# Performance work log

Hardware: AMD Instinct MI355X
Metric: run time of the kernel (lower is better)

Reference implementation:

```python
import jax, jax.numpy as jnp
import numpy as np
import math

B, S, D, H, DH = 2, 4096, 1024, 16, 64
CHUNK, RNDS, NBUCK, MLP = 128, 2, 64, 4096


def setup_inputs() -> dict:
    key = jax.random.key(0)
    ks = jax.random.split(key, 8)
    return {
        "inputs": jax.random.normal(ks[0], (B, S, D), jnp.float32),
        "ln1_scale": jnp.ones((D,), jnp.float32),
        "ln1_bias": jnp.zeros((D,), jnp.float32),
        "w_qk": jax.random.normal(ks[1], (D, H, DH), jnp.float32) * 0.02,
        "w_v": jax.random.normal(ks[2], (D, H, DH), jnp.float32) * 0.02,
        "w_out": jax.random.normal(ks[3], (H, DH, D), jnp.float32) * 0.02,
        "rotations": jax.random.normal(ks[4], (DH, RNDS, NBUCK // 2), jnp.float32),
        "ln2_scale": jnp.ones((D,), jnp.float32),
        "ln2_bias": jnp.zeros((D,), jnp.float32),
        "w_mlp1": jax.random.normal(ks[5], (D, MLP), jnp.float32) * 0.02,
        "b_mlp1": jnp.zeros((MLP,), jnp.float32),
        "w_mlp2": jax.random.normal(ks[6], (MLP, D), jnp.float32) * 0.02,
        "b_mlp2": jnp.zeros((D,), jnp.float32),
    }


def _layer_norm(x, scale, bias):
    mu = x.mean(-1, keepdims=True)
    var = ((x - mu) ** 2).mean(-1, keepdims=True)
    return (x - mu) / jnp.sqrt(var + 1e-6) * scale + bias


def _attend_one(q, k, v, buckets):
    # q,k,v: [S,DH]; buckets: [S] int. Sort by bucket (stable via position tiebreak),
    # chunk, attend to own chunk + 1 before + 1 after (look_both_side).
    nC = S // CHUNK
    order = jnp.argsort(buckets * S + jnp.arange(S))  # [S]
    undo = jnp.argsort(order)
    sq = q[order].reshape(nC, CHUNK, DH)
    sk = k[order].reshape(nC, CHUNK, DH)
    sv = v[order].reshape(nC, CHUNK, DH)
    st = order.reshape(nC, CHUNK)  # original token positions
    look = lambda x: jnp.concatenate([x, jnp.roll(x, 1, axis=0), jnp.roll(x, -1, axis=0)], axis=1)
    bk, bv = look(sk), look(sv)
    bt = look(st[..., None])[..., 0]
    dots = jnp.einsum('nqd,nkd->nqk', sq, bk) / math.sqrt(DH)
    # self_mask: a token attends to itself only if nothing else is available
    dots = dots - 1e5 * (st[:, :, None] == bt[:, None, :]).astype(dots.dtype)
    slog = jax.nn.logsumexp(dots, axis=-1)           # [nC,CHUNK]
    o = jnp.einsum('nqk,nkd->nqd', jax.nn.softmax(dots, axis=-1), bv)
    return o.reshape(S, DH)[undo], slog.reshape(S)[undo]


def _lsh_attention(qk, v, rotations):
    # qk,v: [B,H,S,DH]; shared-QK Reformer attention; keys are length-normalized.
    xn = qk / (jnp.linalg.norm(qk, axis=-1, keepdims=True) + 1e-6)
    rot = jnp.einsum('bhsd,drm->bhrsm', xn, rotations)          # [B,H,R,S,NBUCK/2]
    buckets = jnp.argmax(jnp.concatenate([rot, -rot], -1), -1)  # [B,H,R,S]
    rep = lambda x: jnp.broadcast_to(x[:, :, None], (B, H, RNDS, S, DH)).reshape(-1, S, DH)
    o, slog = jax.vmap(_attend_one)(rep(qk), rep(xn), rep(v), buckets.reshape(-1, S))
    o = o.reshape(B, H, RNDS, S, DH)
    slog = slog.reshape(B, H, RNDS, S)
    w = jax.nn.softmax(slog, axis=2)  # combine hash rounds by their logsumexp weight
    return (o * w[..., None]).sum(axis=2)  # [B,H,S,DH]


def reference(inputs, ln1_scale, ln1_bias, w_qk, w_v, w_out, rotations,
              ln2_scale, ln2_bias, w_mlp1, b_mlp1, w_mlp2, b_mlp2):
    x = _layer_norm(inputs, ln1_scale, ln1_bias)
    qk = jnp.einsum('bsd,dhe->bhse', x, w_qk)
    v = jnp.einsum('bsd,dhe->bhse', x, w_v)
    att = _lsh_attention(qk, v, rotations)
    x2 = inputs + jnp.einsum('bhse,hed->bsd', att, w_out)
    y = _layer_norm(x2, ln2_scale, ln2_bias)
    y = jax.nn.gelu(y @ w_mlp1 + b_mlp1) @ w_mlp2 + b_mlp2
    return x2 + y
```

## Files before the change

kernel.cpp:

```cpp
#include <hip/hip_runtime.h>
#include <hip/hip_bf16.h>


typedef short short8 __attribute__((ext_vector_type(8)));
typedef float f32x4 __attribute__((ext_vector_type(4)));
typedef unsigned short us4 __attribute__((ext_vector_type(4)));

__device__ __forceinline__ unsigned short f2bf(float f) {
  unsigned u = __builtin_bit_cast(unsigned, f);
  u += 0x7FFFu + ((u >> 16) & 1u);
  return (unsigned short)(u >> 16);
}

__device__ __forceinline__ float bf2f(unsigned short u) {
  return __builtin_bit_cast(float, ((unsigned)u) << 16);
}

__device__ __forceinline__ float gelu_f(float x) {
  float x3 = x * x * x;
  float t = tanhf(0.7978845608028654f * (x + 0.044715f * x3));
  return 0.5f * x * (1.0f + t);
}

__device__ __forceinline__ void load_lds16(const void* g, void* l) {
  __builtin_amdgcn_global_load_lds(
      (const __attribute__((address_space(1))) unsigned int*)g,
      (__attribute__((address_space(3))) unsigned int*)l, 16, 0, 0);
}

__global__ __launch_bounds__(256) void transpose_cast(
    const float* __restrict__ in, unsigned short* __restrict__ out, int R,
    int C) {
  __shared__ float tile[32][33];
  int ctiles = C >> 5;
  int bx = blockIdx.x % ctiles;
  int by = blockIdx.x / ctiles;
  int tx = threadIdx.x & 31;
  int ty = threadIdx.x >> 5;
#pragma unroll
  for (int i = 0; i < 32; i += 8)
    tile[ty + i][tx] = in[(size_t)(by * 32 + ty + i) * C + bx * 32 + tx];
  __syncthreads();
#pragma unroll
  for (int i = 0; i < 32; i += 8)
    out[(size_t)(bx * 32 + ty + i) * R + by * 32 + tx] = f2bf(tile[tx][ty + i]);
}

__global__ __launch_bounds__(256) void ln_bf16(const float* __restrict__ x,
                                               const float* __restrict__ sc,
                                               const float* __restrict__ bi,
                                               unsigned short* __restrict__ y) {
  int row = blockIdx.x, tid = threadIdx.x, lane = tid & 63, wv = tid >> 6;
  const float* xr = x + (size_t)row * 1024;
  float4 v = *(const float4*)(xr + tid * 4);
  float s1 = v.x + v.y + v.z + v.w;
  float s2 = v.x * v.x + v.y * v.y + v.z * v.z + v.w * v.w;
#pragma unroll
  for (int o = 1; o < 64; o <<= 1) {
    s1 += __shfl_xor(s1, o);
    s2 += __shfl_xor(s2, o);
  }
  __shared__ float a1[4], a2[4];
  if (lane == 0) {
    a1[wv] = s1;
    a2[wv] = s2;
  }
  __syncthreads();
  s1 = a1[0] + a1[1] + a1[2] + a1[3];
  s2 = a2[0] + a2[1] + a2[2] + a2[3];
  float mu = s1 * (1.f / 1024.f);
  float var = s2 * (1.f / 1024.f) - mu * mu;
  float rs = rsqrtf(var + 1e-6f);
  int c = tid * 4;
  us4 o4;
  o4.x = f2bf((v.x - mu) * rs * sc[c + 0] + bi[c + 0]);
  o4.y = f2bf((v.y - mu) * rs * sc[c + 1] + bi[c + 1]);
  o4.z = f2bf((v.z - mu) * rs * sc[c + 2] + bi[c + 2]);
  o4.w = f2bf((v.w - mu) * rs * sc[c + 3] + bi[c + 3]);
  *(us4*)(y + (size_t)row * 1024 + c) = o4;
}


template <int BK, int EPI>
__global__ __launch_bounds__(256) void gemm_bt(
    const unsigned short* __restrict__ A, const unsigned short* __restrict__ Bt,
    const float* __restrict__ bias, const float* __restrict__ res,
    float* __restrict__ Cf, unsigned short* __restrict__ Cb,
    unsigned short* __restrict__ Cb2, int M, int N, int K) {
  constexpr int GR = BK / 8;
  constexpr int RPS = 2048 / BK;
  constexpr int LPM = BK / 16;

  __shared__ unsigned short sA[2][128 * BK];
  __shared__ unsigned short sB[2][128 * BK];

  const int nbx = N / 128;
  const int nwg = gridDim.x;
  const int cpx = nwg >> 3;
  const int bid = blockIdx.x;
  const int swz = (bid & 7) * cpx + (bid >> 3);
  const int bx = swz % nbx;
  const int by = swz / nbx;
  const int tid = threadIdx.x;
  const int lane = tid & 63;
  const int wave = tid >> 6;
  const int wr = wave >> 1, wc = wave & 1;
  const int l15 = lane & 15;
  const int lhi = lane >> 4;

  const int srow = tid / GR;
  const int swzrow = (BK == 32) ? ((srow >> 1) & 3) : (srow & 7);
  const int sgl = (tid % GR) ^ swzrow;
  const unsigned short* Ag = A + (size_t)(by * 128 + srow) * K + sgl * 8;
  const unsigned short* Bg = Bt + (size_t)(bx * 128 + srow) * K + sgl * 8;

  f32x4 acc[4][4];
#pragma unroll
  for (int m = 0; m < 4; ++m)
#pragma unroll
    for (int n = 0; n < 4; ++n) {
      f32x4 z = {0.f, 0.f, 0.f, 0.f};
      acc[m][n] = z;
    }

  const int KT = K / BK;

  auto STAGE = [&](int ktile, int buf) {
    const unsigned short* As = Ag + (size_t)ktile * BK;
    const unsigned short* Bs = Bg + (size_t)ktile * BK;
#pragma unroll
    for (int i = 0; i < LPM; ++i) {
      load_lds16(As + (size_t)i * RPS * K,
                 (char*)&sA[buf][0] + tid * 16 + i * 4096);
      load_lds16(Bs + (size_t)i * RPS * K,
                 (char*)&sB[buf][0] + tid * 16 + i * 4096);
    }
  };

  STAGE(0, 0);
  __syncthreads();

  int cur = 0;
  const int arow = wr * 64 + l15;
  const int brow = wc * 64 + l15;

  for (int kt = 0; kt < KT; ++kt) {
    if (kt + 1 < KT) STAGE(kt + 1, cur ^ 1);
#pragma unroll
    for (int ks = 0; ks < BK / 32; ++ks) {
      const int physg =
          (BK == 32) ? (lhi ^ ((l15 >> 1) & 3)) : ((ks * 4 + lhi) ^ (l15 & 7));
      const int koff = physg * 8;
      short8 af[4], bfv[4];
#pragma unroll
      for (int m = 0; m < 4; ++m)
        af[m] = *(const short8*)&sA[cur][(arow + m * 16) * BK + koff];
#pragma unroll
      for (int n = 0; n < 4; ++n)
        bfv[n] = *(const short8*)&sB[cur][(brow + n * 16) * BK + koff];
#pragma unroll
      for (int m = 0; m < 4; ++m)
#pragma unroll
        for (int n = 0; n < 4; ++n)
          acc[m][n] = __builtin_amdgcn_mfma_f32_16x16x32_bf16(
              af[m], bfv[n], acc[m][n], 0, 0, 0);
    }
    __syncthreads();
    cur ^= 1;
  }

  const int r0 = by * 128 + wr * 64;
  const int c0 = bx * 128 + wc * 64;
#pragma unroll
  for (int m = 0; m < 4; ++m) {
#pragma unroll
    for (int n = 0; n < 4; ++n) {
#pragma unroll
      for (int i = 0; i < 4; ++i) {
        int rr = r0 + m * 16 + lhi * 4 + i;
        int cc = c0 + n * 16 + l15;
        float vacc = acc[m][n][i];
        if (EPI == 1) {
          float t = vacc + bias[cc];
          Cb[(size_t)rr * N + cc] = f2bf(gelu_f(t));
        } else if (EPI == 2) {
          float t = vacc + res[(size_t)rr * N + cc];
          if (bias != nullptr) t += bias[cc];
          Cf[(size_t)rr * N + cc] = t;
        } else if (EPI == 5) {
          if (cc < 1024) {
            Cf[(size_t)rr * 1024 + cc] = vacc;
            Cb[(size_t)rr * 1024 + cc] = f2bf(vacc);
          } else {
            Cb2[(size_t)rr * 1024 + (cc - 1024)] = f2bf(vacc);
          }
        }
      }
    }
  }
}

__global__ __launch_bounds__(256) void bucket_kernel(
    const float* __restrict__ qk, const float* __restrict__ rot,
    unsigned short* __restrict__ knb, int* __restrict__ buckets) {
  __shared__ float rotl[64 * 64];
  __shared__ float xnl[4][64];
  int tid = threadIdx.x, lane = tid & 63, wv = tid >> 6;
  for (int i = tid; i < 4096; i += 256) rotl[i] = rot[i];
  __syncthreads();
  for (int it = 0; it < 8; ++it) {
    int g = (it * 4096 + blockIdx.x) * 4 + wv;
    int bh = g >> 12;
    int s = g & 4095;
    int b = bh >> 4, h = bh & 15;
    size_t rowoff = (size_t)(b * 4096 + s) * 1024 + h * 64;
    float x = qk[rowoff + lane];
    float ss = x * x;
#pragma unroll
    for (int o = 1; o < 64; o <<= 1) ss += __shfl_xor(ss, o);
    float rn = 1.f / (sqrtf(ss) + 1e-6f);
    float xn = x * rn;
    knb[rowoff + lane] = f2bf(xn);
    xnl[wv][lane] = xn;
    __syncthreads();
    int r_ = lane >> 5, m_ = lane & 31;
    float a = 0.f;
#pragma unroll 16
    for (int d = 0; d < 64; ++d) a += xnl[wv][d] * rotl[d * 64 + r_ * 32 + m_];
    float bv;
    int bi;
    if (a >= 0.f) {
      bv = a;
      bi = m_;
    } else {
      bv = -a;
      bi = m_ + 32;
    }
#pragma unroll
    for (int o = 16; o >= 1; o >>= 1) {
      float ov = __shfl_xor(bv, o);
      int oi = __shfl_xor(bi, o);
      if (ov > bv || (ov == bv && oi < bi)) {
        bv = ov;
        bi = oi;
      }
    }
    if (m_ == 0) buckets[((size_t)bh * 2 + r_) * 4096 + s] = bi;
    __syncthreads();
  }
}

#define HSTR 65

__global__ __launch_bounds__(256) void sort_kernel(
    const int* __restrict__ buckets, int* __restrict__ order) {
  __shared__ unsigned int hist[256 * HSTR];
  __shared__ unsigned int bucketStart[64];
  const int bhr = blockIdx.x;
  const int t = threadIdx.x;
  const int* bk = buckets + (size_t)bhr * 4096;

  unsigned int* hrow = &hist[t * HSTR];
#pragma unroll
  for (int b = 0; b < 64; ++b) hrow[b] = 0u;

  int bks[16];
  {
    const int4* bp = (const int4*)(bk + t * 16);
#pragma unroll
    for (int j4 = 0; j4 < 4; ++j4) {
      int4 v = bp[j4];
      bks[j4 * 4 + 0] = v.x;
      bks[j4 * 4 + 1] = v.y;
      bks[j4 * 4 + 2] = v.z;
      bks[j4 * 4 + 3] = v.w;
    }
  }
#pragma unroll
  for (int j = 0; j < 16; ++j) hrow[bks[j]]++;
  __syncthreads();

  if (t < 64) {
    unsigned int acc = 0;
    for (int t2 = 0; t2 < 256; ++t2) {
      unsigned int c = hist[t2 * HSTR + t];
      hist[t2 * HSTR + t] = acc;
      acc += c;
    }
    bucketStart[t] = acc;
  }
  __syncthreads();
  if (t == 0) {
    unsigned int acc = 0;
    for (int b = 0; b < 64; ++b) {
      unsigned int c = bucketStart[b];
      bucketStart[b] = acc;
      acc += c;
    }
  }
  __syncthreads();

  int* op = order + (size_t)bhr * 4096;
#pragma unroll
  for (int j = 0; j < 16; ++j) {
    int b = bks[j];
    unsigned int pos = bucketStart[b] + hrow[b];
    hrow[b]++;
    op[pos] = t * 16 + j;
  }
}

#define KSTR 72
#define PSTR 136

__global__ __launch_bounds__(256, 2) void lsh_attn_mfma(
    const unsigned short* __restrict__ qb, const unsigned short* __restrict__ knb,
    const unsigned short* __restrict__ vb, const int* __restrict__ order,
    unsigned short* __restrict__ ob, float* __restrict__ slog) {
  __shared__ unsigned short Kls[128 * KSTR];
  __shared__ unsigned short Vt[64 * PSTR];
  __shared__ unsigned short Pls[4][32 * PSTR];
  __shared__ int qtokL[128];
  __shared__ int btok[128];

  const int bid = blockIdx.x;
  const int swz = (bid & 7) * 256 + (bid >> 3);
  const int c = swz & 31;
  const int bhr = swz >> 5;
  const int bh = bhr >> 1;
  const int h = bh & 15, b = bh >> 4;
  const int* ord = order + (size_t)bhr * 4096;
  const int tid = threadIdx.x, lane = tid & 63, wv = tid >> 6;
  const int l15 = lane & 15, lhi = lane >> 4;

  if (tid < 128) qtokL[tid] = ord[c * 128 + tid];
  __syncthreads();

  short8 qf[2][2];
#pragma unroll
  for (int mt = 0; mt < 2; ++mt) {
#pragma unroll
    for (int ks = 0; ks < 2; ++ks) {
      int tok = qtokL[wv * 32 + mt * 16 + l15];
      qf[mt][ks] = *(const short8*)(qb + (size_t)(b * 4096 + tok) * 1024 +
                                    h * 64 + ks * 32 + lhi * 8);
    }
  }

  float mrun[2][4], lrun[2][4];
  f32x4 oacc[2][4];
#pragma unroll
  for (int mt = 0; mt < 2; ++mt)
#pragma unroll
    for (int i = 0; i < 4; ++i) {
      mrun[mt][i] = -1e30f;
      lrun[mt][i] = 0.f;
    }
#pragma unroll
  for (int mt = 0; mt < 2; ++mt)
#pragma unroll
    for (int n = 0; n < 4; ++n) {
      f32x4 z = {0.f, 0.f, 0.f, 0.f};
      oacc[mt][n] = z;
    }

  for (int st = 0; st < 3; ++st) {
    int kc = (st == 0) ? c : (st == 1) ? ((c + 31) & 31) : ((c + 1) & 31);
    __syncthreads();
    {
      int row = tid >> 1, half = tid & 1;
      int ktok = ord[kc * 128 + row];
      if (half == 0) btok[row] = ktok;
      size_t rowoff = (size_t)(b * 4096 + ktok) * 1024 + h * 64 + half * 32;
      const short8* kp = (const short8*)(knb + rowoff);
      const short8* vp = (const short8*)(vb + rowoff);
#pragma unroll
      for (int i = 0; i < 4; ++i)
        *(short8*)&Kls[row * KSTR + half * 32 + i * 8] = kp[i];
#pragma unroll
      for (int i = 0; i < 4; ++i) {
        short8 vw = vp[i];
        int d0 = half * 32 + i * 8;
#pragma unroll
        for (int j = 0; j < 8; ++j)
          Vt[(d0 + j) * PSTR + row] = (unsigned short)vw[j];
      }
    }
    __syncthreads();

    f32x4 sacc[2][8];
#pragma unroll
    for (int mt = 0; mt < 2; ++mt)
#pragma unroll
      for (int n = 0; n < 8; ++n) {
        f32x4 z = {0.f, 0.f, 0.f, 0.f};
        sacc[mt][n] = z;
      }
#pragma unroll
    for (int ks = 0; ks < 2; ++ks) {
      short8 kf[8];
#pragma unroll
      for (int n = 0; n < 8; ++n)
        kf[n] = *(const short8*)&Kls[(n * 16 + l15) * KSTR + ks * 32 + lhi * 8];
#pragma unroll
      for (int mt = 0; mt < 2; ++mt)
#pragma unroll
        for (int n = 0; n < 8; ++n)
          sacc[mt][n] = __builtin_amdgcn_mfma_f32_16x16x32_bf16(
              qf[mt][ks], kf[n], sacc[mt][n], 0, 0, 0);
    }

    int ktA[8];
#pragma unroll
    for (int n = 0; n < 8; ++n) ktA[n] = btok[n * 16 + l15];
#pragma unroll
    for (int mt = 0; mt < 2; ++mt) {
#pragma unroll
      for (int i = 0; i < 4; ++i) {
        int qrow = wv * 32 + mt * 16 + lhi * 4 + i;
        int qt = qtokL[qrow];
        float sv[8];
        float mx = -1e30f;
#pragma unroll
        for (int n = 0; n < 8; ++n) {
          float s = sacc[mt][n][i] * 0.125f;
          if (ktA[n] == qt) s -= 1e5f;
          sv[n] = s;
          mx = fmaxf(mx, s);
        }
#pragma unroll
        for (int d = 1; d < 16; d <<= 1) mx = fmaxf(mx, __shfl_xor(mx, d));
        float mold = mrun[mt][i];
        float mnew = fmaxf(mold, mx);
        float scl = __expf(mold - mnew);
        lrun[mt][i] *= scl;
#pragma unroll
        for (int n = 0; n < 4; ++n) oacc[mt][n][i] *= scl;
        float ps = 0.f;
#pragma unroll
        for (int n = 0; n < 8; ++n) {
          float p = __expf(sv[n] - mnew);
          ps += p;
          Pls[wv][(mt * 16 + lhi * 4 + i) * PSTR + n * 16 + l15] = f2bf(p);
        }
#pragma unroll
        for (int d = 1; d < 16; d <<= 1) ps += __shfl_xor(ps, d);
        lrun[mt][i] = lrun[mt][i] + ps;
        mrun[mt][i] = mnew;
      }
    }

#pragma unroll
    for (int ks = 0; ks < 4; ++ks) {
      short8 pf[2];
#pragma unroll
      for (int mt = 0; mt < 2; ++mt)
        pf[mt] =
            *(const short8*)&Pls[wv][(mt * 16 + l15) * PSTR + ks * 32 + lhi * 8];
      short8 vfr[4];
#pragma unroll
      for (int n = 0; n < 4; ++n)
        vfr[n] = *(const short8*)&Vt[(n * 16 + l15) * PSTR + ks * 32 + lhi * 8];
#pragma unroll
      for (int mt = 0; mt < 2; ++mt)
#pragma unroll
        for (int n = 0; n < 4; ++n)
          oacc[mt][n] = __builtin_amdgcn_mfma_f32_16x16x32_bf16(
              pf[mt], vfr[n], oacc[mt][n], 0, 0, 0);
    }
  }

#pragma unroll
  for (int mt = 0; mt < 2; ++mt) {
#pragma unroll
    for (int i = 0; i < 4; ++i) {
      int qrow = wv * 32 + mt * 16 + lhi * 4 + i;
      int tok = qtokL[qrow];
      float l = lrun[mt][i];
      float invl = 1.f / l;
      if (l15 == 0) slog[(size_t)bhr * 4096 + tok] = logf(l) + mrun[mt][i];
      unsigned short* orow = ob + ((size_t)bhr * 4096 + tok) * 64;
#pragma unroll
      for (int n = 0; n < 4; ++n)
        orow[n * 16 + l15] = f2bf(oacc[mt][n][i] * invl);
    }
  }
}

__global__ __launch_bounds__(256) void combine_rounds(
    const unsigned short* __restrict__ ob, const float* __restrict__ slog,
    unsigned short* __restrict__ att) {
  int g = blockIdx.x * 4 + (threadIdx.x >> 6);
  int lane = threadIdx.x & 63;
  int h = g & 15;
  int bs = g >> 4;
  int b = bs >> 12;
  int s = bs & 4095;
  size_t base = ((size_t)(b * 16 + h) * 2) * 4096 + s;
  size_t i0 = base;
  size_t i1 = base + 4096;
  float s0 = slog[i0], s1 = slog[i1];
  float mx = fmaxf(s0, s1);
  float e0 = __expf(s0 - mx), e1 = __expf(s1 - mx);
  float w0 = e0 / (e0 + e1);
  float w1 = 1.f - w0;
  float v0 = bf2f(ob[i0 * 64 + lane]);
  float v1 = bf2f(ob[i1 * 64 + lane]);
  att[(size_t)bs * 1024 + h * 64 + lane] = f2bf(w0 * v0 + w1 * v1);
}

extern "C" void kernel_launch(void* const* d_in, const int* in_sizes, int n_in,
                              void* d_out, int out_size, void* d_ws,
                              size_t ws_size, hipStream_t stream) {
  const float* inputs = (const float*)d_in[0];
  const float* ln1s = (const float*)d_in[1];
  const float* ln1b = (const float*)d_in[2];
  const float* wqk = (const float*)d_in[3];
  const float* wv = (const float*)d_in[4];
  const float* wout = (const float*)d_in[5];
  const float* rot = (const float*)d_in[6];
  const float* ln2s = (const float*)d_in[7];
  const float* ln2b = (const float*)d_in[8];
  const float* wm1 = (const float*)d_in[9];
  const float* bm1 = (const float*)d_in[10];
  const float* wm2 = (const float*)d_in[11];
  const float* bm2 = (const float*)d_in[12];

  char* w = (char*)d_ws;
  auto alloc = [&](size_t bytes) {
    char* p = w;
    w += (bytes + 255) & ~(size_t)255;
    return p;
  };
  unsigned short* wqkv_bt = (unsigned short*)alloc(2048ull * 1024 * 2);
  unsigned short* wout_bt = (unsigned short*)alloc(1024ull * 1024 * 2);
  unsigned short* wm1_bt = (unsigned short*)alloc(4096ull * 1024 * 2);
  unsigned short* wm2_bt = (unsigned short*)alloc(1024ull * 4096 * 2);
  unsigned short* bufA = (unsigned short*)alloc(8192ull * 1024 * 2);
  float* qkf = (float*)alloc(8192ull * 1024 * 4);
  unsigned short* qb = (unsigned short*)alloc(8192ull * 1024 * 2);
  unsigned short* knb = (unsigned short*)alloc(8192ull * 1024 * 2);
  unsigned short* vb = (unsigned short*)alloc(8192ull * 1024 * 2);
  int* buckets = (int*)alloc(64ull * 4096 * 4);
  int* order = (int*)alloc(64ull * 4096 * 4);
  unsigned short* big =
      (unsigned short*)alloc(8192ull * 4096 * 2);
  float* slogb = (float*)alloc(64ull * 4096 * 4);
  float* x2 = qkf;
  unsigned short* obuf = big;
  unsigned short* h1 = big;

  transpose_cast<<<32 * 32, 256, 0, stream>>>(wqk, wqkv_bt, 1024, 1024);
  transpose_cast<<<32 * 32, 256, 0, stream>>>(wv, wqkv_bt + 1024ull * 1024,
                                              1024, 1024);
  transpose_cast<<<32 * 32, 256, 0, stream>>>(wout, wout_bt, 1024, 1024);
  transpose_cast<<<32 * 128, 256, 0, stream>>>(wm1, wm1_bt, 1024, 4096);
  transpose_cast<<<128 * 32, 256, 0, stream>>>(wm2, wm2_bt, 4096, 1024);

  ln_bf16<<<8192, 256, 0, stream>>>(inputs, ln1s, ln1b, bufA);

  gemm_bt<64, 5><<<64 * 16, 256, 0, stream>>>(bufA, wqkv_bt, nullptr, nullptr,
                                              qkf, qb, vb, 8192, 2048, 1024);

  bucket_kernel<<<4096, 256, 0, stream>>>(qkf, rot, knb, buckets);
  sort_kernel<<<64, 256, 0, stream>>>(buckets, order);
  lsh_attn_mfma<<<2048, 256, 0, stream>>>(qb, knb, vb, order, obuf, slogb);
  combine_rounds<<<32768, 256, 0, stream>>>(obuf, slogb, bufA);

  gemm_bt<64, 2><<<64 * 8, 256, 0, stream>>>(bufA, wout_bt, nullptr, inputs,
                                             x2, nullptr, nullptr, 8192, 1024,
                                             1024);
  ln_bf16<<<8192, 256, 0, stream>>>(x2, ln2s, ln2b, bufA);
  gemm_bt<32, 1><<<64 * 32, 256, 0, stream>>>(bufA, wm1_bt, bm1, nullptr,
                                              nullptr, h1, nullptr, 8192, 4096,
                                              1024);
  gemm_bt<64, 2><<<64 * 8, 256, 0, stream>>>(h1, wm2_bt, bm2, x2,
                                             (float*)d_out, nullptr, nullptr,
                                             8192, 1024, 4096);
}
```

Before: 497.8 us.

## Add phased-pipeline GEMM with split LDS reads and fine-grained waits

```diff
diff --git a/kernel.cpp b/kernel.cpp
--- a/kernel.cpp
+++ b/kernel.cpp
@@ -17,9 +17,8 @@
 }
 
 __device__ __forceinline__ float gelu_f(float x) {
-  float x3 = x * x * x;
-  float t = tanhf(0.7978845608028654f * (x + 0.044715f * x3));
-  return 0.5f * x * (1.0f + t);
+  float y = 1.5957691216057308f * (x + 0.044715f * x * x * x);
+  return x / (1.f + __expf(-y));
 }
 
 __device__ __forceinline__ void load_lds16(const void* g, void* l) {
@@ -80,20 +79,14 @@
   *(us4*)(y + (size_t)row * 1024 + c) = o4;
 }
 
-
-template <int BK, int EPI>
+template <int EPI>
 __global__ __launch_bounds__(256) void gemm_bt(
     const unsigned short* __restrict__ A, const unsigned short* __restrict__ Bt,
     const float* __restrict__ bias, const float* __restrict__ res,
-    float* __restrict__ Cf, unsigned short* __restrict__ Cb,
-    unsigned short* __restrict__ Cb2, int M, int N, int K) {
-  constexpr int GR = BK / 8;
-  constexpr int RPS = 2048 / BK;
-  constexpr int LPM = BK / 16;
-
-  __shared__ unsigned short sA[2][128 * BK];
-  __shared__ unsigned short sB[2][128 * BK];
-
+    float* __restrict__ Cf, unsigned short* __restrict__ Cb, int M, int N,
+    int K) {
+  __shared__ unsigned short sA[2][128 * 32];
+  __shared__ unsigned short sB[2][128 * 32];
   const int nbx = N / 128;
   const int nwg = gridDim.x;
   const int cpx = nwg >> 3;
@@ -108,9 +101,8 @@
   const int l15 = lane & 15;
   const int lhi = lane >> 4;
 
-  const int srow = tid / GR;
-  const int swzrow = (BK == 32) ? ((srow >> 1) & 3) : (srow & 7);
-  const int sgl = (tid % GR) ^ swzrow;
+  const int srow = tid >> 2;
+  const int sgl = (tid & 3) ^ ((srow >> 1) & 3);
   const unsigned short* Ag = A + (size_t)(by * 128 + srow) * K + sgl * 8;
   const unsigned short* Bg = Bt + (size_t)(bx * 128 + srow) * K + sgl * 8;
 
@@ -123,16 +115,16 @@
       acc[m][n] = z;
     }
 
-  const int KT = K / BK;
+  const int KT = K / 32;
 
   auto STAGE = [&](int ktile, int buf) {
-    const unsigned short* As = Ag + (size_t)ktile * BK;
-    const unsigned short* Bs = Bg + (size_t)ktile * BK;
-#pragma unroll
-    for (int i = 0; i < LPM; ++i) {
-      load_lds16(As + (size_t)i * RPS * K,
+    const unsigned short* As = Ag + (size_t)ktile * 32;
+    const unsigned short* Bs = Bg + (size_t)ktile * 32;
+#pragma unroll
+    for (int i = 0; i < 2; ++i) {
+      load_lds16(As + (size_t)i * 64 * K,
                  (char*)&sA[buf][0] + tid * 16 + i * 4096);
-      load_lds16(Bs + (size_t)i * RPS * K,
+      load_lds16(Bs + (size_t)i * 64 * K,
                  (char*)&sB[buf][0] + tid * 16 + i * 4096);
     }
   };
@@ -143,28 +135,23 @@
   int cur = 0;
   const int arow = wr * 64 + l15;
   const int brow = wc * 64 + l15;
+  const int koff = (lhi ^ ((l15 >> 1) & 3)) * 8;
 
   for (int kt = 0; kt < KT; ++kt) {
     if (kt + 1 < KT) STAGE(kt + 1, cur ^ 1);
-#pragma unroll
-    for (int ks = 0; ks < BK / 32; ++ks) {
-      const int physg =
-          (BK == 32) ? (lhi ^ ((l15 >> 1) & 3)) : ((ks * 4 + lhi) ^ (l15 & 7));
-      const int koff = physg * 8;
-      short8 af[4], bfv[4];
-#pragma unroll
-      for (int m = 0; m < 4; ++m)
-        af[m] = *(const short8*)&sA[cur][(arow + m * 16) * BK + koff];
+    short8 af[4], bfv[4];
+#pragma unroll
+    for (int m = 0; m < 4; ++m)
+      af[m] = *(const short8*)&sA[cur][(arow + m * 16) * 32 + koff];
+#pragma unroll
+    for (int n = 0; n < 4; ++n)
+      bfv[n] = *(const short8*)&sB[cur][(brow + n * 16) * 32 + koff];
+#pragma unroll
+    for (int m = 0; m < 4; ++m)
 #pragma unroll
       for (int n = 0; n < 4; ++n)
-        bfv[n] = *(const short8*)&sB[cur][(brow + n * 16) * BK + koff];
-#pragma unroll
-      for (int m = 0; m < 4; ++m)
-#pragma unroll
-        for (int n = 0; n < 4; ++n)
-          acc[m][n] = __builtin_amdgcn_mfma_f32_16x16x32_bf16(
-              af[m], bfv[n], acc[m][n], 0, 0, 0);
-    }
+        acc[m][n] = __builtin_amdgcn_mfma_f32_16x16x32_bf16(af[m], bfv[n],
+                                                            acc[m][n], 0, 0, 0);
     __syncthreads();
     cur ^= 1;
   }
@@ -184,6 +171,196 @@
           float t = vacc + bias[cc];
           Cb[(size_t)rr * N + cc] = f2bf(gelu_f(t));
         } else if (EPI == 2) {
+          float t = vacc + res[(size_t)rr * N + cc];
+          if (bias != nullptr) t += bias[cc];
+          Cf[(size_t)rr * N + cc] = t;
+        }
+      }
+    }
+  }
+}
+
+template <int EPI>
+__global__ __launch_bounds__(256) void gemm_p4(
+    const unsigned short* __restrict__ A, const unsigned short* __restrict__ Bt,
+    const float* __restrict__ bias, const float* __restrict__ res,
+    float* __restrict__ Cf, unsigned short* __restrict__ Cb,
+    unsigned short* __restrict__ Cb2, int M, int N, int K) {
+  __shared__ unsigned short sA[2][128 * 64];
+  __shared__ unsigned short sB[2][128 * 64];
+  const int nbx = N / 128;
+  const int nwg = gridDim.x;
+  const int cpx = nwg >> 3;
+  const int bid = blockIdx.x;
+  const int swz = (bid & 7) * cpx + (bid >> 3);
+  const int bx = swz % nbx;
+  const int by = swz / nbx;
+  const int tid = threadIdx.x;
+  const int lane = tid & 63;
+  const int wave = tid >> 6;
+  const int wr = wave >> 1, wc = wave & 1;
+  const int l15 = lane & 15;
+  const int lhi = lane >> 4;
+
+  const int r = tid >> 3;
+  const int g = tid & 7;
+  const int sgl = g ^ (r & 7);
+  const unsigned short* Ag = A + (size_t)(by * 128 + r) * K + sgl * 8;
+  const unsigned short* Bg = Bt + (size_t)(bx * 128 + r) * K + sgl * 8;
+  const int dst = tid * 16;
+
+  f32x4 acc[4][4];
+#pragma unroll
+  for (int m = 0; m < 4; ++m)
+#pragma unroll
+    for (int n = 0; n < 4; ++n) {
+      f32x4 z = {0.f, 0.f, 0.f, 0.f};
+      acc[m][n] = z;
+    }
+
+  const int KT = K / 64;
+
+  auto ISS = [&](int idx, int ktile, int buf) {
+    const int Rs = ((idx >> 2) << 5) + ((idx & 1) << 6);
+    const unsigned short* src =
+        ((idx & 2) ? Bg : Ag) + (size_t)Rs * K + (size_t)ktile * 64;
+    char* d = (char*)((idx & 2) ? &sB[buf][0] : &sA[buf][0]) + Rs * 128 + dst;
+    load_lds16(src, d);
+  };
+
+  const int arowb = wr * 64 + l15;
+  const int browb = wc * 64 + l15;
+  auto readA = [&](int m, int ks, int c) {
+    return *(const short8*)&sA[c][(arowb + m * 16) * 64 +
+                                  (((ks * 4 + lhi) ^ (l15 & 7)) << 3)];
+  };
+  auto readB = [&](int n, int ks, int c) {
+    return *(const short8*)&sB[c][(browb + n * 16) * 64 +
+                                  (((ks * 4 + lhi) ^ (l15 & 7)) << 3)];
+  };
+
+#define WAITV(N_) asm volatile("s_waitcnt vmcnt(" #N_ ")" ::: "memory")
+#define PHASE_SYNC()                              \
+  do {                                            \
+    __builtin_amdgcn_sched_barrier(0);            \
+    __builtin_amdgcn_s_barrier();                 \
+    asm volatile("s_waitcnt lgkmcnt(0)" ::: "memory"); \
+    __builtin_amdgcn_sched_barrier(0);            \
+  } while (0)
+
+#pragma unroll
+  for (int i = 0; i < 8; ++i) ISS(i, 0, 0);
+  WAITV(4);
+  __builtin_amdgcn_sched_barrier(0);
+  __builtin_amdgcn_s_barrier();
+
+  for (int kt = 0; kt < KT; ++kt) {
+    const int c = kt & 1;
+    const bool pre = (kt + 1 < KT);
+    short8 a0[2][2], a1[2][2], b0[2][2], b1[2][2];
+
+#pragma unroll
+    for (int i = 0; i < 2; ++i)
+#pragma unroll
+      for (int ks = 0; ks < 2; ++ks) {
+        a0[i][ks] = readA(i, ks, c);
+        b0[i][ks] = readB(i, ks, c);
+      }
+    if (pre) {
+      ISS(0, kt + 1, c ^ 1);
+      ISS(1, kt + 1, c ^ 1);
+      WAITV(4);
+    } else {
+      WAITV(2);
+    }
+    PHASE_SYNC();
+    __builtin_amdgcn_s_setprio(1);
+#pragma unroll
+    for (int i = 0; i < 2; ++i)
+#pragma unroll
+      for (int n = 0; n < 2; ++n)
+#pragma unroll
+        for (int ks = 0; ks < 2; ++ks)
+          acc[i][n] = __builtin_amdgcn_mfma_f32_16x16x32_bf16(
+              a0[i][ks], b0[n][ks], acc[i][n], 0, 0, 0);
+    __builtin_amdgcn_s_setprio(0);
+
+#pragma unroll
+    for (int i = 0; i < 2; ++i)
+#pragma unroll
+      for (int ks = 0; ks < 2; ++ks) a1[i][ks] = readA(2 + i, ks, c);
+    if (pre) {
+      ISS(2, kt + 1, c ^ 1);
+      ISS(3, kt + 1, c ^ 1);
+      WAITV(4);
+    } else {
+      WAITV(0);
+    }
+    PHASE_SYNC();
+    __builtin_amdgcn_s_setprio(1);
+#pragma unroll
+    for (int i = 0; i < 2; ++i)
+#pragma unroll
+      for (int n = 0; n < 2; ++n)
+#pragma unroll
+        for (int ks = 0; ks < 2; ++ks)
+          acc[2 + i][n] = __builtin_amdgcn_mfma_f32_16x16x32_bf16(
+              a1[i][ks], b0[n][ks], acc[2 + i][n], 0, 0, 0);
+    __builtin_amdgcn_s_setprio(0);
+
+#pragma unroll
+    for (int i = 0; i < 2; ++i)
+#pragma unroll
+      for (int ks = 0; ks < 2; ++ks) b1[i][ks] = readB(2 + i, ks, c);
+    if (pre) {
+      ISS(4, kt + 1, c ^ 1);
+      ISS(5, kt + 1, c ^ 1);
+      WAITV(4);
+    }
+    PHASE_SYNC();
+    __builtin_amdgcn_s_setprio(1);
+#pragma unroll
+    for (int i = 0; i < 2; ++i)
+#pragma unroll
+      for (int n = 0; n < 2; ++n)
+#pragma unroll
+        for (int ks = 0; ks < 2; ++ks)
+          acc[2 + i][2 + n] = __builtin_amdgcn_mfma_f32_16x16x32_bf16(
+              a1[i][ks], b1[n][ks], acc[2 + i][2 + n], 0, 0, 0);
+    __builtin_amdgcn_s_setprio(0);
+
+    if (pre) {
+      ISS(6, kt + 1, c ^ 1);
+      ISS(7, kt + 1, c ^ 1);
+      WAITV(4);
+    }
+    PHASE_SYNC();
+    __builtin_amdgcn_s_setprio(1);
+#pragma unroll
+    for (int i = 0; i < 2; ++i)
+#pragma unroll
+      for (int n = 0; n < 2; ++n)
+#pragma unroll
+        for (int ks = 0; ks < 2; ++ks)
+          acc[i][2 + n] = __builtin_amdgcn_mfma_f32_16x16x32_bf16(
+              a0[i][ks], b1[n][ks], acc[i][2 + n], 0, 0, 0);
+    __builtin_amdgcn_s_setprio(0);
+  }
+#undef WAITV
+#undef PHASE_SYNC
+
+  const int r0 = by * 128 + wr * 64;
+  const int c0 = bx * 128 + wc * 64;
+#pragma unroll
+  for (int m = 0; m < 4; ++m) {
+#pragma unroll
+    for (int n = 0; n < 4; ++n) {
+#pragma unroll
+      for (int i = 0; i < 4; ++i) {
+        int rr = r0 + m * 16 + lhi * 4 + i;
+        int cc = c0 + n * 16 + l15;
+        float vacc = acc[m][n][i];
+        if (EPI == 2) {
           float t = vacc + res[(size_t)rr * N + cc];
           if (bias != nullptr) t += bias[cc];
           Cf[(size_t)rr * N + cc] = t;
@@ -559,22 +736,19 @@
 
   ln_bf16<<<8192, 256, 0, stream>>>(inputs, ln1s, ln1b, bufA);
 
-  gemm_bt<64, 5><<<64 * 16, 256, 0, stream>>>(bufA, wqkv_bt, nullptr, nullptr,
-                                              qkf, qb, vb, 8192, 2048, 1024);
+  gemm_p4<5><<<64 * 16, 256, 0, stream>>>(bufA, wqkv_bt, nullptr, nullptr, qkf,
+                                          qb, vb, 8192, 2048, 1024);
 
   bucket_kernel<<<4096, 256, 0, stream>>>(qkf, rot, knb, buckets);
   sort_kernel<<<64, 256, 0, stream>>>(buckets, order);
   lsh_attn_mfma<<<2048, 256, 0, stream>>>(qb, knb, vb, order, obuf, slogb);
   combine_rounds<<<32768, 256, 0, stream>>>(obuf, slogb, bufA);
 
-  gemm_bt<64, 2><<<64 * 8, 256, 0, stream>>>(bufA, wout_bt, nullptr, inputs,
-                                             x2, nullptr, nullptr, 8192, 1024,
-                                             1024);
+  gemm_p4<2><<<64 * 8, 256, 0, stream>>>(bufA, wout_bt, nullptr, inputs, x2,
+                                         nullptr, nullptr, 8192, 1024, 1024);
   ln_bf16<<<8192, 256, 0, stream>>>(x2, ln2s, ln2b, bufA);
-  gemm_bt<32, 1><<<64 * 32, 256, 0, stream>>>(bufA, wm1_bt, bm1, nullptr,
-                                              nullptr, h1, nullptr, 8192, 4096,
-                                              1024);
-  gemm_bt<64, 2><<<64 * 8, 256, 0, stream>>>(h1, wm2_bt, bm2, x2,
-                                             (float*)d_out, nullptr, nullptr,
-                                             8192, 1024, 4096);
-}
+  gemm_bt<1><<<64 * 32, 256, 0, stream>>>(bufA, wm1_bt, bm1, nullptr, nullptr,
+                                          h1, 8192, 4096, 1024);
+  gemm_p4<2><<<64 * 8, 256, 0, stream>>>(h1, wm2_bt, bm2, x2, (float*)d_out,
+                                         nullptr, nullptr, 8192, 1024, 4096);
+}
```

New measurement: 514.6 us. 1.03x slower.

## Add 256x256 eight-wave GEMM with staged LDS prefetch for QKV and MLP1

Applied to the files above, without the earlier changes.

```diff
diff --git a/kernel.cpp b/kernel.cpp
--- a/kernel.cpp
+++ b/kernel.cpp
@@ -17,9 +17,8 @@
 }
 
 __device__ __forceinline__ float gelu_f(float x) {
-  float x3 = x * x * x;
-  float t = tanhf(0.7978845608028654f * (x + 0.044715f * x3));
-  return 0.5f * x * (1.0f + t);
+  float y = 1.5957691216057308f * (x + 0.044715f * x * x * x);
+  return x / (1.f + __expf(-y));
 }
 
 __device__ __forceinline__ void load_lds16(const void* g, void* l) {
@@ -80,20 +79,14 @@
   *(us4*)(y + (size_t)row * 1024 + c) = o4;
 }
 
-
-template <int BK, int EPI>
+template <int EPI>
 __global__ __launch_bounds__(256) void gemm_bt(
     const unsigned short* __restrict__ A, const unsigned short* __restrict__ Bt,
     const float* __restrict__ bias, const float* __restrict__ res,
-    float* __restrict__ Cf, unsigned short* __restrict__ Cb,
-    unsigned short* __restrict__ Cb2, int M, int N, int K) {
-  constexpr int GR = BK / 8;
-  constexpr int RPS = 2048 / BK;
-  constexpr int LPM = BK / 16;
-
-  __shared__ unsigned short sA[2][128 * BK];
-  __shared__ unsigned short sB[2][128 * BK];
-
+    float* __restrict__ Cf, unsigned short* __restrict__ Cb, int M, int N,
+    int K) {
+  __shared__ unsigned short sA[2][128 * 64];
+  __shared__ unsigned short sB[2][128 * 64];
   const int nbx = N / 128;
   const int nwg = gridDim.x;
   const int cpx = nwg >> 3;
@@ -108,9 +101,8 @@
   const int l15 = lane & 15;
   const int lhi = lane >> 4;
 
-  const int srow = tid / GR;
-  const int swzrow = (BK == 32) ? ((srow >> 1) & 3) : (srow & 7);
-  const int sgl = (tid % GR) ^ swzrow;
+  const int srow = tid >> 3;
+  const int sgl = (tid & 7) ^ (srow & 7);
   const unsigned short* Ag = A + (size_t)(by * 128 + srow) * K + sgl * 8;
   const unsigned short* Bg = Bt + (size_t)(bx * 128 + srow) * K + sgl * 8;
 
@@ -123,16 +115,16 @@
       acc[m][n] = z;
     }
 
-  const int KT = K / BK;
+  const int KT = K / 64;
 
   auto STAGE = [&](int ktile, int buf) {
-    const unsigned short* As = Ag + (size_t)ktile * BK;
-    const unsigned short* Bs = Bg + (size_t)ktile * BK;
-#pragma unroll
-    for (int i = 0; i < LPM; ++i) {
-      load_lds16(As + (size_t)i * RPS * K,
+    const unsigned short* As = Ag + (size_t)ktile * 64;
+    const unsigned short* Bs = Bg + (size_t)ktile * 64;
+#pragma unroll
+    for (int i = 0; i < 4; ++i) {
+      load_lds16(As + (size_t)i * 32 * K,
                  (char*)&sA[buf][0] + tid * 16 + i * 4096);
-      load_lds16(Bs + (size_t)i * RPS * K,
+      load_lds16(Bs + (size_t)i * 32 * K,
                  (char*)&sB[buf][0] + tid * 16 + i * 4096);
     }
   };
@@ -147,17 +139,15 @@
   for (int kt = 0; kt < KT; ++kt) {
     if (kt + 1 < KT) STAGE(kt + 1, cur ^ 1);
 #pragma unroll
-    for (int ks = 0; ks < BK / 32; ++ks) {
-      const int physg =
-          (BK == 32) ? (lhi ^ ((l15 >> 1) & 3)) : ((ks * 4 + lhi) ^ (l15 & 7));
-      const int koff = physg * 8;
+    for (int ks = 0; ks < 2; ++ks) {
+      const int koff = (((ks * 4 + lhi) ^ (l15 & 7)) << 3);
       short8 af[4], bfv[4];
 #pragma unroll
       for (int m = 0; m < 4; ++m)
-        af[m] = *(const short8*)&sA[cur][(arow + m * 16) * BK + koff];
+        af[m] = *(const short8*)&sA[cur][(arow + m * 16) * 64 + koff];
 #pragma unroll
       for (int n = 0; n < 4; ++n)
-        bfv[n] = *(const short8*)&sB[cur][(brow + n * 16) * BK + koff];
+        bfv[n] = *(const short8*)&sB[cur][(brow + n * 16) * 64 + koff];
 #pragma unroll
       for (int m = 0; m < 4; ++m)
 #pragma unroll
@@ -180,13 +170,194 @@
         int rr = r0 + m * 16 + lhi * 4 + i;
         int cc = c0 + n * 16 + l15;
         float vacc = acc[m][n][i];
-        if (EPI == 1) {
-          float t = vacc + bias[cc];
-          Cb[(size_t)rr * N + cc] = f2bf(gelu_f(t));
-        } else if (EPI == 2) {
+        if (EPI == 2) {
           float t = vacc + res[(size_t)rr * N + cc];
           if (bias != nullptr) t += bias[cc];
           Cf[(size_t)rr * N + cc] = t;
+        }
+      }
+    }
+  }
+}
+
+template <int EPI>
+__global__ __launch_bounds__(512, 2) void gemm_8p(
+    const unsigned short* __restrict__ A, const unsigned short* __restrict__ Bt,
+    const float* __restrict__ bias, float* __restrict__ Cf,
+    unsigned short* __restrict__ Cb, unsigned short* __restrict__ Cb2, int M,
+    int N, int K) {
+  __shared__ unsigned short sA[2][256 * 64];
+  __shared__ unsigned short sB[2][256 * 64];
+  const int nbx = N >> 8;
+  const int nwg = gridDim.x;
+  const int cpx = nwg >> 3;
+  const int bid = blockIdx.x;
+  const int swz = (bid & 7) * cpx + (bid >> 3);
+  const int bx = swz % nbx;
+  const int by = swz / nbx;
+  const int tid = threadIdx.x;
+  const int lane = tid & 63;
+  const int wid = tid >> 6;
+  const int wr = wid >> 2;
+  const int wc = wid & 3;
+  const int l15 = lane & 15;
+  const int lhi = lane >> 4;
+
+  const int sr = tid >> 3;
+  const int sgl = (tid & 7) ^ (sr & 7);
+  const unsigned short* Ab = A + ((size_t)(by * 256) + sr) * K + sgl * 8;
+  const unsigned short* Bb = Bt + ((size_t)(bx * 256) + sr) * K + sgl * 8;
+
+  f32x4 acc[8][4];
+#pragma unroll
+  for (int m = 0; m < 8; ++m)
+#pragma unroll
+    for (int n = 0; n < 4; ++n) {
+      f32x4 z = {0.f, 0.f, 0.f, 0.f};
+      acc[m][n] = z;
+    }
+
+  const int KT = K >> 6;
+
+  auto ISSUE = [&](int mat, int half, int kt, int buf) {
+    const unsigned short* src =
+        (mat ? Bb : Ab) + (size_t)(half * 128) * K + kt * 64;
+    char* d =
+        (char*)(mat ? &sB[buf][0] : &sA[buf][0]) + half * 16384 + tid * 16;
+    load_lds16(src, d);
+    load_lds16(src + (size_t)64 * K, d + 8192);
+  };
+
+  auto rdA = [&](int m, int ks, int c) {
+    int row = ((m & 4) << 5) + wr * 64 + ((m & 3) << 4) + l15;
+    int pg = ((ks << 2) + lhi) ^ (l15 & 7);
+    return *(const short8*)&sA[c][row * 64 + pg * 8];
+  };
+  auto rdB = [&](int n, int ks, int c) {
+    int row = ((n & 2) << 6) + wc * 32 + ((n & 1) << 4) + l15;
+    int pg = ((ks << 2) + lhi) ^ (l15 & 7);
+    return *(const short8*)&sB[c][row * 64 + pg * 8];
+  };
+
+#define PRE_MFMA()                                   \
+  __builtin_amdgcn_sched_barrier(0);                 \
+  __builtin_amdgcn_s_barrier();                      \
+  asm volatile("s_waitcnt lgkmcnt(0)" ::: "memory"); \
+  __builtin_amdgcn_sched_barrier(0);                 \
+  __builtin_amdgcn_s_setprio(1)
+#define POST_MFMA()                \
+  __builtin_amdgcn_s_setprio(0);   \
+  __builtin_amdgcn_sched_barrier(0); \
+  __builtin_amdgcn_s_barrier()
+
+  ISSUE(0, 0, 0, 0);
+  ISSUE(1, 0, 0, 0);
+  ISSUE(0, 1, 0, 0);
+  ISSUE(1, 1, 0, 0);
+  asm volatile("s_waitcnt vmcnt(4)" ::: "memory");
+  if (KT > 1) {
+    ISSUE(0, 0, 1, 1);
+    ISSUE(1, 0, 1, 1);
+    ISSUE(0, 1, 1, 1);
+  }
+  asm volatile("s_waitcnt vmcnt(6)" ::: "memory");
+  __builtin_amdgcn_sched_barrier(0);
+  __builtin_amdgcn_s_barrier();
+
+  for (int kt = 0; kt < KT; ++kt) {
+    const int c = kt & 1;
+    short8 a0[4][2], a1[4][2], b0[2][2], b1[2][2];
+
+#pragma unroll
+    for (int m = 0; m < 4; ++m)
+#pragma unroll
+      for (int ks = 0; ks < 2; ++ks) a0[m][ks] = rdA(m, ks, c);
+#pragma unroll
+    for (int n = 0; n < 2; ++n)
+#pragma unroll
+      for (int ks = 0; ks < 2; ++ks) b0[n][ks] = rdB(n, ks, c);
+    if (kt + 1 < KT) ISSUE(1, 1, kt + 1, c ^ 1);
+    PRE_MFMA();
+#pragma unroll
+    for (int m = 0; m < 4; ++m)
+#pragma unroll
+      for (int n = 0; n < 2; ++n)
+#pragma unroll
+        for (int ks = 0; ks < 2; ++ks)
+          acc[m][n] = __builtin_amdgcn_mfma_f32_16x16x32_bf16(
+              a0[m][ks], b0[n][ks], acc[m][n], 0, 0, 0);
+    POST_MFMA();
+
+#pragma unroll
+    for (int m = 0; m < 4; ++m)
+#pragma unroll
+      for (int ks = 0; ks < 2; ++ks) a1[m][ks] = rdA(4 + m, ks, c);
+    if (kt + 2 < KT) ISSUE(0, 0, kt + 2, c);
+    PRE_MFMA();
+#pragma unroll
+    for (int m = 0; m < 4; ++m)
+#pragma unroll
+      for (int n = 0; n < 2; ++n)
+#pragma unroll
+        for (int ks = 0; ks < 2; ++ks)
+          acc[4 + m][n] = __builtin_amdgcn_mfma_f32_16x16x32_bf16(
+              a1[m][ks], b0[n][ks], acc[4 + m][n], 0, 0, 0);
+    POST_MFMA();
+
+#pragma unroll
+    for (int n = 0; n < 2; ++n)
+#pragma unroll
+      for (int ks = 0; ks < 2; ++ks) b1[n][ks] = rdB(2 + n, ks, c);
+    if (kt + 2 < KT) ISSUE(1, 0, kt + 2, c);
+    PRE_MFMA();
+#pragma unroll
+    for (int m = 0; m < 4; ++m)
+#pragma unroll
+      for (int n = 0; n < 2; ++n)
+#pragma unroll
+        for (int ks = 0; ks < 2; ++ks)
+          acc[4 + m][2 + n] = __builtin_amdgcn_mfma_f32_16x16x32_bf16(
+              a1[m][ks], b1[n][ks], acc[4 + m][2 + n], 0, 0, 0);
+    POST_MFMA();
+
+    if (kt + 2 < KT) ISSUE(0, 1, kt + 2, c);
+    __builtin_amdgcn_s_setprio(1);
+#pragma unroll
+    for (int m = 0; m < 4; ++m)
+#pragma unroll
+      for (int n = 0; n < 2; ++n)
+#pragma unroll
+        for (int ks = 0; ks < 2; ++ks)
+          acc[m][2 + n] = __builtin_amdgcn_mfma_f32_16x16x32_bf16(
+              a0[m][ks], b1[n][ks], acc[m][2 + n], 0, 0, 0);
+    __builtin_amdgcn_s_setprio(0);
+    if (kt + 1 < KT) {
+      if (kt + 2 < KT) {
+        asm volatile("s_waitcnt vmcnt(6)" ::: "memory");
+      } else {
+        asm volatile("s_waitcnt vmcnt(0)" ::: "memory");
+      }
+      __builtin_amdgcn_sched_barrier(0);
+      __builtin_amdgcn_s_barrier();
+    }
+  }
+#undef PRE_MFMA
+#undef POST_MFMA
+
+  const int r0 = by * 256 + wr * 64;
+  const int c0 = bx * 256 + wc * 32;
+#pragma unroll
+  for (int m = 0; m < 8; ++m) {
+    const int rb = r0 + ((m & 4) << 5) + ((m & 3) << 4) + lhi * 4;
+#pragma unroll
+    for (int n = 0; n < 4; ++n) {
+      const int cc = c0 + ((n & 2) << 6) + ((n & 1) << 4) + l15;
+#pragma unroll
+      for (int i = 0; i < 4; ++i) {
+        const int rr = rb + i;
+        float vacc = acc[m][n][i];
+        if (EPI == 1) {
+          Cb[(size_t)rr * N + cc] = f2bf(gelu_f(vacc + bias[cc]));
         } else if (EPI == 5) {
           if (cc < 1024) {
             Cf[(size_t)rr * 1024 + cc] = vacc;
@@ -559,22 +730,19 @@
 
   ln_bf16<<<8192, 256, 0, stream>>>(inputs, ln1s, ln1b, bufA);
 
-  gemm_bt<64, 5><<<64 * 16, 256, 0, stream>>>(bufA, wqkv_bt, nullptr, nullptr,
-                                              qkf, qb, vb, 8192, 2048, 1024);
+  gemm_8p<5><<<32 * 8, 512, 0, stream>>>(bufA, wqkv_bt, nullptr, qkf, qb, vb,
+                                         8192, 2048, 1024);
 
   bucket_kernel<<<4096, 256, 0, stream>>>(qkf, rot, knb, buckets);
   sort_kernel<<<64, 256, 0, stream>>>(buckets, order);
   lsh_attn_mfma<<<2048, 256, 0, stream>>>(qb, knb, vb, order, obuf, slogb);
   combine_rounds<<<32768, 256, 0, stream>>>(obuf, slogb, bufA);
 
-  gemm_bt<64, 2><<<64 * 8, 256, 0, stream>>>(bufA, wout_bt, nullptr, inputs,
-                                             x2, nullptr, nullptr, 8192, 1024,
-                                             1024);
+  gemm_bt<2><<<64 * 8, 256, 0, stream>>>(bufA, wout_bt, nullptr, inputs, x2,
+                                         nullptr, 8192, 1024, 1024);
   ln_bf16<<<8192, 256, 0, stream>>>(x2, ln2s, ln2b, bufA);
-  gemm_bt<32, 1><<<64 * 32, 256, 0, stream>>>(bufA, wm1_bt, bm1, nullptr,
-                                              nullptr, h1, nullptr, 8192, 4096,
-                                              1024);
-  gemm_bt<64, 2><<<64 * 8, 256, 0, stream>>>(h1, wm2_bt, bm2, x2,
-                                             (float*)d_out, nullptr, nullptr,
-                                             8192, 1024, 4096);
-}
+  gemm_8p<1><<<32 * 16, 512, 0, stream>>>(bufA, wm1_bt, bm1, nullptr, h1,
+                                          nullptr, 8192, 4096, 1024);
+  gemm_bt<2><<<64 * 8, 256, 0, stream>>>(h1, wm2_bt, bm2, x2, (float*)d_out,
+                                         nullptr, 8192, 1024, 4096);
+}
```

Result: faster. 471.4 us (-5.3%).
